# Kernel optimization log

Measured on AMD Instinct MI355X. Metric: run time of the kernel, lower is better.

## Reference

```python
import jax, jax.numpy as jnp
import numpy as np

NUM_HEADS = 4

def gelu(x):
    # torch nn.GELU() default is the exact (erf) form
    return jax.nn.gelu(x, approximate=False)

def setup_inputs() -> dict:
    key = jax.random.key(0)
    k0, k1, k2, k3, k4 = jax.random.split(key, 5)
    B, N, F, T = 2, 2048, 64, 12
    hidden = 32
    d = hidden // NUM_HEADS  # 8
    x = jax.random.normal(k0, (B, N, F, T), dtype=jnp.float32)
    adj = jax.random.uniform(k1, (N, N), dtype=jnp.float32)
    w1 = jax.random.normal(k2, (T,), dtype=jnp.float32) * 0.1          # W_mapping1 (out=1)
    W2 = jax.random.normal(k3, (F, hidden), dtype=jnp.float32) * 0.1   # W_mapping2
    a = jax.random.normal(k4, (2 * d + 1,), dtype=jnp.float32) * 0.1   # A_mapping (out=1)
    return {"x": x, "adj": adj, "w1": w1, "W2": W2, "a": a}

def reference(x, adj, w1, W2, a):
    H = NUM_HEADS
    B, N, F, T = x.shape
    # W_mapping1 + squeeze + GELU: (B,N,F)
    q = gelu(jnp.einsum('bnft,t->bnf', x, w1))
    # W_mapping2: (B,N,hidden)
    Q = jnp.einsum('bnf,fh->bnh', q, W2)
    hid = Q.shape[-1]
    d = hid // H
    Q4 = Q.reshape(B, N, H, d)  # per-head features
    aq, ak, aadj = a[:d], a[d:2 * d], a[2 * d]
    # A_mapping(cat(Q,K,adj)) is linear => decompose into scalar projections.
    # K[b,i,j] = Q[b,j] (permute of broadcast Q), so:
    sq = jnp.einsum('bnhd,d->bnh', Q4, aq)  # (B,N,H) query-node term
    sk = jnp.einsum('bnhd,d->bnh', Q4, ak)  # (B,N,H) key-node term
    # scores[b,i,j,h] = GELU(sq[b,i,h] + sk[b,j,h] + adj[i,j]*aadj)
    scores = gelu(sq[:, :, None, :] + sk[:, None, :, :] + adj[None, :, :, None] * aadj)
    return scores.transpose(0, 3, 1, 2)  # (B, H, N, N)
```

## Files before the change

### kernel.cpp

```cpp
#include <hip/hip_runtime.h>
#include <math.h>

#define NH 4
#define DH 8
#define NF 64
#define NT 12
#define NB 2
#define IT 4

__device__ __forceinline__ float gelu_f(float x) {
    const float s = x * 0.70710678118654752440f;
    const float z = __builtin_fabsf(s);
    const float t = __builtin_amdgcn_rcpf(fmaf(0.3275911f, z, 1.0f));
    float p = fmaf(1.061405429f, t, -1.453152027f);
    p = fmaf(p, t, 1.421413741f);
    p = fmaf(p, t, -0.284496736f);
    p = fmaf(p, t, 0.254829592f);
    p *= t;
    const float e = __builtin_amdgcn_exp2f(z * z * -1.44269504088896340736f);
    const float erfa = fmaf(-p, e, 1.0f);
    const float erfv = __builtin_copysignf(erfa, s);
    return 0.5f * x * (1.0f + erfv);
}

__global__ __launch_bounds__(256) void qk_kernel(
    const float* __restrict__ x, const float* __restrict__ w1,
    const float* __restrict__ W2, const float* __restrict__ a,
    float* __restrict__ sqT, float* __restrict__ skT, int N)
{
    __shared__ float Wq[NF][NH + 1];
    __shared__ float Wk[NF][NH + 1];
    const int t = threadIdx.x;

    {
        int f = t >> 2, h = t & 3;
        float accq = 0.f, acck = 0.f;
        #pragma unroll
        for (int k = 0; k < DH; ++k) {
            float w = W2[f * (NH * DH) + h * DH + k];
            accq += w * a[k];
            acck += w * a[DH + k];
        }
        Wq[f][h] = accq;
        Wk[f][h] = acck;
    }
    __syncthreads();

    float w1r[NT];
    #pragma unroll
    for (int i = 0; i < NT; ++i) w1r[i] = w1[i];

    const int wave = t >> 6;
    const int lane = t & 63;
    const long long row = (long long)blockIdx.x * 4 + wave;
    if (row >= (long long)NB * N) return;

    const float* xr = x + row * (NF * NT) + (long long)lane * NT;
    float4 v0 = *(const float4*)(xr);
    float4 v1 = *(const float4*)(xr + 4);
    float4 v2 = *(const float4*)(xr + 8);
    float dot = v0.x*w1r[0] + v0.y*w1r[1] + v0.z*w1r[2]  + v0.w*w1r[3]
              + v1.x*w1r[4] + v1.y*w1r[5] + v1.z*w1r[6]  + v1.w*w1r[7]
              + v2.x*w1r[8] + v2.y*w1r[9] + v2.z*w1r[10] + v2.w*w1r[11];
    float q = gelu_f(dot);

    float acc[8];
    #pragma unroll
    for (int h = 0; h < NH; ++h) {
        acc[h]     = q * Wq[lane][h];
        acc[4 + h] = q * Wk[lane][h];
    }
    #pragma unroll
    for (int ofs = 32; ofs > 0; ofs >>= 1) {
        #pragma unroll
        for (int i = 0; i < 8; ++i)
            acc[i] += __shfl_xor(acc[i], ofs, 64);
    }
    if (lane < 8) {
        int h   = lane & 3;
        int isK = lane >> 2;
        int b   = (int)(row / N);
        int n   = (int)(row % N);
        float* dst = isK ? skT : sqT;
        dst[((long long)b * NH + h) * N + n] = acc[lane];
    }
}

__global__ __launch_bounds__(256) void score_kernel_lds(
    const float* __restrict__ adj, const float* __restrict__ sqT,
    const float* __restrict__ skT, const float* __restrict__ a,
    float* __restrict__ out, int N)
{
    const float aadj = a[2 * DH];
    const int t   = threadIdx.x;
    const int nq  = N >> 2;
    const int wpr = nq >> 8;
    const int ig  = blockIdx.x / wpr;
    const int w   = blockIdx.x - ig * wpr;
    const int i0  = ig * IT;
    const int q0  = w << 8;

    __shared__ float adjS[IT][1024];

    #pragma unroll
    for (int r = 0; r < IT; ++r) {
        float4 v = *(const float4*)(adj + (long long)(i0 + r) * N + ((q0 + t) << 2));
        float4 sv; sv.x = v.x * aadj; sv.y = v.y * aadj;
                   sv.z = v.z * aadj; sv.w = v.w * aadj;
        *(float4*)&adjS[r][t << 2] = sv;
    }
    __syncthreads();

    const int wave = t >> 6;
    const int lane = t & 63;

    #pragma unroll
    for (int bb = 0; bb < 2; ++bb) {
        const int bh = (wave << 1) + bb;

        float4 sk[4];
        #pragma unroll
        for (int k = 0; k < 4; ++k)
            sk[k] = *(const float4*)(skT + (long long)bh * N + ((q0 + lane + (k << 6)) << 2));

        #pragma unroll
        for (int ii = 0; ii < IT; ++ii) {
            const float sq = sqT[(long long)bh * N + i0 + ii];
            #pragma unroll
            for (int k = 0; k < 4; ++k) {
                const int qw = lane + (k << 6);
                const float* ar = &adjS[ii][qw << 2];
                float4 o;
                o.x = gelu_f(sq + sk[k].x + ar[0]);
                o.y = gelu_f(sq + sk[k].y + ar[1]);
                o.z = gelu_f(sq + sk[k].z + ar[2]);
                o.w = gelu_f(sq + sk[k].w + ar[3]);
                *(float4*)(out + ((long long)bh * N + i0 + ii) * N + ((q0 + qw) << 2)) = o;
            }
        }
    }
}

__global__ __launch_bounds__(256) void score_kernel_flat(
    const float* __restrict__ adj, const float* __restrict__ sqT,
    const float* __restrict__ skT, const float* __restrict__ a,
    float* __restrict__ out, int N)
{
    const float aadj = a[2 * DH];
    const int nq = N >> 2;
    long long tid = (long long)blockIdx.x * blockDim.x + threadIdx.x;
    if (tid >= (long long)N * nq) return;
    const int i  = (int)(tid / nq);
    const int j0 = (int)(tid % nq) << 2;

    float4 adj4 = *(const float4*)(adj + (long long)i * N + j0);
    const float a0 = adj4.x * aadj;
    const float a1 = adj4.y * aadj;
    const float a2 = adj4.z * aadj;
    const float a3 = adj4.w * aadj;

    #pragma unroll
    for (int bh = 0; bh < NB * NH; ++bh) {
        const float sq = sqT[(long long)bh * N + i];
        float4 sk4 = *(const float4*)(skT + (long long)bh * N + j0);
        float4 o;
        o.x = gelu_f(sq + sk4.x + a0);
        o.y = gelu_f(sq + sk4.y + a1);
        o.z = gelu_f(sq + sk4.z + a2);
        o.w = gelu_f(sq + sk4.w + a3);
        *(float4*)(out + ((long long)bh * N + i) * N + j0) = o;
    }
}

extern "C" void kernel_launch(void* const* d_in, const int* in_sizes, int n_in,
                              void* d_out, int out_size, void* d_ws, size_t ws_size,
                              hipStream_t stream)
{
    const float* x   = (const float*)d_in[0];
    const float* adj = (const float*)d_in[1];
    const float* w1  = (const float*)d_in[2];
    const float* W2  = (const float*)d_in[3];
    const float* a   = (const float*)d_in[4];
    float* out = (float*)d_out;

    int N = 1;
    while ((long long)(N + 1) * (N + 1) <= (long long)in_sizes[1]) ++N;

    float* sqT = (float*)d_ws;
    float* skT = sqT + (size_t)NB * NH * N;

    const int rows = NB * N;
    qk_kernel<<<(rows + 3) / 4, 256, 0, stream>>>(x, w1, W2, a, sqT, skT, N);

    const int nq = N >> 2;
    if ((nq & 255) == 0 && (N % IT) == 0) {
        const int wpr = nq >> 8;
        const int blocks = (N / IT) * wpr;
        score_kernel_lds<<<blocks, 256, 0, stream>>>(adj, sqT, skT, a, out, N);
    } else {
        const long long total = (long long)N * nq;
        score_kernel_flat<<<(int)((total + 255) / 256), 256, 0, stream>>>(adj, sqT, skT, a, out, N);
    }
}
```

Baseline: 34.36 us.

## Map each wave to one batch-head with full-row tiles in the score kernel

The score kernel now launches 512-thread blocks that each cover IT full adjacency rows, and each of the 8 waves handles one (batch, head) pair across the whole row width. The scaled adjacency rows go into dynamic shared memory. Each adj element is read once per 4 rows and shared across all 8 batch-heads, instead of being reloaded for every 1024-column chunk. This yields fewer, larger blocks (512 instead of 1024) with 32 KB of LDS each, which may reduce occupancy. The fast path is hard-coded for N == 2048.

```diff
diff --git a/kernel.cpp b/kernel.cpp
--- a/kernel.cpp
+++ b/kernel.cpp
@@ -86,56 +86,53 @@
     }
 }
 
-__global__ __launch_bounds__(256) void score_kernel_lds(
+__global__ __launch_bounds__(512) void score_kernel_wavebh(
     const float* __restrict__ adj, const float* __restrict__ sqT,
     const float* __restrict__ skT, const float* __restrict__ a,
     float* __restrict__ out, int N)
 {
     const float aadj = a[2 * DH];
-    const int t   = threadIdx.x;
-    const int nq  = N >> 2;
-    const int wpr = nq >> 8;
-    const int ig  = blockIdx.x / wpr;
-    const int w   = blockIdx.x - ig * wpr;
-    const int i0  = ig * IT;
-    const int q0  = w << 8;
-
-    __shared__ float adjS[IT][1024];
+    const int t  = threadIdx.x;
+    const int i0 = (int)blockIdx.x * IT;
+
+    extern __shared__ float adjS[];
 
     #pragma unroll
     for (int r = 0; r < IT; ++r) {
-        float4 v = *(const float4*)(adj + (long long)(i0 + r) * N + ((q0 + t) << 2));
+        float4 v = *(const float4*)(adj + (long long)(i0 + r) * N + (t << 2));
         float4 sv; sv.x = v.x * aadj; sv.y = v.y * aadj;
                    sv.z = v.z * aadj; sv.w = v.w * aadj;
-        *(float4*)&adjS[r][t << 2] = sv;
+        *(float4*)&adjS[r * N + (t << 2)] = sv;
     }
     __syncthreads();
 
     const int wave = t >> 6;
     const int lane = t & 63;
-
-    #pragma unroll
-    for (int bb = 0; bb < 2; ++bb) {
-        const int bh = (wave << 1) + bb;
-
-        float4 sk[4];
+    const int nq   = N >> 2;
+    const int KQ   = nq >> 6;
+
+    float4 sk[8];
+    #pragma unroll
+    for (int k = 0; k < 8; ++k) {
+        if (k < KQ)
+            sk[k] = *(const float4*)(skT + (long long)wave * N + ((lane + (k << 6)) << 2));
+    }
+
+    #pragma unroll
+    for (int ii = 0; ii < IT; ++ii) {
+        const float sq = sqT[(long long)wave * N + i0 + ii];
+        float* orow = out + ((long long)wave * N + i0 + ii) * N;
         #pragma unroll
-        for (int k = 0; k < 4; ++k)
-            sk[k] = *(const float4*)(skT + (long long)bh * N + ((q0 + lane + (k << 6)) << 2));
-
-        #pragma unroll
-        for (int ii = 0; ii < IT; ++ii) {
-            const float sq = sqT[(long long)bh * N + i0 + ii];
-            #pragma unroll
-            for (int k = 0; k < 4; ++k) {
+        for (int k = 0; k < 8; ++k) {
+            if (k < KQ) {
                 const int qw = lane + (k << 6);
-                const float* ar = &adjS[ii][qw << 2];
+                const float* ar = &adjS[ii * N + (qw << 2)];
                 float4 o;
                 o.x = gelu_f(sq + sk[k].x + ar[0]);
                 o.y = gelu_f(sq + sk[k].y + ar[1]);
                 o.z = gelu_f(sq + sk[k].z + ar[2]);
                 o.w = gelu_f(sq + sk[k].w + ar[3]);
-                *(float4*)(out + ((long long)bh * N + i0 + ii) * N + ((q0 + qw) << 2)) = o;
+                *(float4*)(orow + (qw << 2)) = o;
             }
         }
     }
@@ -192,12 +189,11 @@
     const int rows = NB * N;
     qk_kernel<<<(rows + 3) / 4, 256, 0, stream>>>(x, w1, W2, a, sqT, skT, N);
 
-    const int nq = N >> 2;
-    if ((nq & 255) == 0 && (N % IT) == 0) {
-        const int wpr = nq >> 8;
-        const int blocks = (N / IT) * wpr;
-        score_kernel_lds<<<blocks, 256, 0, stream>>>(adj, sqT, skT, a, out, N);
+    if (N == 2048) {
+        const size_t ldsBytes = (size_t)IT * N * sizeof(float);
+        score_kernel_wavebh<<<N / IT, 512, ldsBytes, stream>>>(adj, sqT, skT, a, out, N);
     } else {
+        const int nq = N >> 2;
         const long long total = (long long)N * nq;
         score_kernel_flat<<<(int)((total + 255) / 256), 256, 0, stream>>>(adj, sqT, skT, a, out, N);
     }
```

Measured after the change: 37.09 us. 8.0% more time.
